# Kernel optimization log

Measured on AMD Instinct MI355X. Metric: run time of the kernel, lower is better.

## Reference

```python
import jax, jax.numpy as jnp
import numpy as np

B, R, C, COILS, SEGS, POL, PAD = 4, 256, 256, 32, 4, 2, 20


def _fft2c(x):
    # centered 2D FFT over axes (1,2) with 1/sqrt(R*C) norm (matches fft2c_coil_tf_buda)
    scale = 1.0 / np.sqrt(x.shape[1] * x.shape[2]).astype(np.float32)
    x = jnp.fft.fftshift(x, axes=(1, 2))
    x = jnp.fft.fft2(x, axes=(1, 2))
    return jnp.fft.fftshift(x, axes=(1, 2)) * scale


def _ifft2c(x):
    # centered 2D IFFT over axes (1,2) with sqrt(R*C) norm (matches ifft2c_coil_tf_buda)
    scale = np.sqrt(x.shape[1] * x.shape[2]).astype(np.float32)
    x = jnp.fft.ifftshift(x, axes=(1, 2))
    x = jnp.fft.ifft2(x, axes=(1, 2))
    return jnp.fft.ifftshift(x, axes=(1, 2)) * scale


def _center_crop(x, h, w):
    oh = (x.shape[1] - h) // 2
    ow = (x.shape[2] - w) // 2
    return x[:, oh:oh + h, ow:ow + w]


def _center_pad(x, h, w):
    ph = h - x.shape[1]
    pw = w - x.shape[2]
    pads = [(0, 0), (ph // 2, ph - ph // 2), (pw // 2, pw - pw // 2), (0, 0)]
    return jnp.pad(x, pads)


def setup_inputs() -> dict:
    key = jax.random.key(0)
    ks = jax.random.split(key, 7)
    return {
        "x_re": jax.random.normal(ks[0], (B, R + PAD, C + PAD, POL), jnp.float32),
        "x_im": jax.random.normal(ks[1], (B, R + PAD, C + PAD, POL), jnp.float32),
        "csm_re": jax.random.normal(ks[2], (B, R, C, COILS), jnp.float32),
        "csm_im": jax.random.normal(ks[3], (B, R, C, COILS), jnp.float32),
        "wmap_re": jax.random.normal(ks[4], (B, R, C, POL, SEGS), jnp.float32),
        "wmap_im": jax.random.normal(ks[5], (B, R, C, POL, SEGS), jnp.float32),
        "mask": jax.random.randint(ks[6], (B, R, C, POL, SEGS), 0, 2).astype(jnp.float32),
        "num_rows": R, "num_cols": C, "num_coils": COILS,
        "num_segs": SEGS, "num_polarities": POL,
    }


def reference(x_re, x_im, csm_re, csm_im, wmap_re, wmap_im, mask,
              num_rows, num_cols, num_coils, num_segs, num_polarities):
    x = (x_re + 1j * x_im).astype(jnp.complex64)
    csm = (csm_re + 1j * csm_im).astype(jnp.complex64)      # [B,R,C,coil]
    wmap = (wmap_re + 1j * wmap_im).astype(jnp.complex64)   # [B,R,C,pol,seg]

    # ---- forward model A ----
    img = _center_crop(x, num_rows, num_cols)                # [B,R,C,pol]
    # broadcast instead of tf.tile: [B,R,C,coil,pol,seg]
    tmp_i = (img[:, :, :, None, :, None]
             * wmap[:, :, :, None, :, :]
             * csm[:, :, :, :, None, None])
    tmp_k = _fft2c(tmp_i)
    kspace = jnp.sum(tmp_k * mask[:, :, :, None, :, :], axis=-1)  # [B,R,C,coil,pol]

    # ---- adjoint model A^H ----
    tk = kspace[..., None] * mask[:, :, :, None, :, :]       # [B,R,C,coil,pol,seg]
    ti = _ifft2c(tk)
    ti = ti * jnp.conj(wmap)[:, :, :, None, :, :] * jnp.conj(csm)[:, :, :, :, None, None]
    out = jnp.sum(ti, axis=(3, 5))                           # sum coils and segments -> [B,R,C,pol]

    out = _center_pad(out, num_rows + PAD, num_rows + PAD)   # tf pads both dims with num_rows+20
    return jnp.stack([out.real, out.imag], axis=-1)          # [B,R+20,R+20,pol,2]
```

## Files before the change

### kernel.cpp

```cpp
#include <hip/hip_runtime.h>
#include <hip/hip_fp16.h>

#define NB 4
#define NR 256
#define NC 256
#define NCOIL 32
#define NSEG 4
#define NPOL 2
#define OD 276
#define OFF 10
#define NCC 16

typedef float2 c32;

__device__ __forceinline__ c32 cmul(c32 a, c32 b){
  return make_float2(a.x*b.x - a.y*b.y, a.x*b.y + a.y*b.x);
}
__device__ __forceinline__ c32 cmulj(c32 a, c32 b){
  return make_float2(a.x*b.x + a.y*b.y, a.y*b.x - a.x*b.y);
}
__device__ __forceinline__ int pd(int a){ return a + (a >> 4); }

__device__ __forceinline__ void wsync(){ __builtin_amdgcn_wave_barrier(); }

__device__ __forceinline__ void init_tab(c32* tab, int tid){
  float th = (float)tid * 0.0245436926061703f;
  float sn, cs;
  sincosf(th, &sn, &cs);
  tab[tid] = make_float2(cs, -sn);
}

template<int DIR>
__device__ __forceinline__ void fft256(const c32* xin, c32* xout,
                                       c32* b0, c32* b1, const c32* tab, int u){
  c32* bufs[2] = { b0, b1 };
  #pragma unroll
  for (int s = 0; s < 4; ++s){
    const int m = 1 << (2*s);
    c32 a0, a1, a2, a3;
    if (s == 0){ a0 = xin[0]; a1 = xin[1]; a2 = xin[2]; a3 = xin[3]; }
    else {
      const c32* src = bufs[(s+1)&1];
      a0 = src[pd(u)]; a1 = src[pd(u+64)]; a2 = src[pd(u+128)]; a3 = src[pd(u+192)];
    }
    c32 s0 = make_float2(a0.x+a2.x, a0.y+a2.y);
    c32 d0 = make_float2(a0.x-a2.x, a0.y-a2.y);
    c32 s1 = make_float2(a1.x+a3.x, a1.y+a3.y);
    c32 d1 = make_float2(a1.x-a3.x, a1.y-a3.y);
    c32 X0 = make_float2(s0.x+s1.x, s0.y+s1.y);
    c32 X2 = make_float2(s0.x-s1.x, s0.y-s1.y);
    c32 X1, X3;
    if (DIR > 0){
      X1 = make_float2(d0.x + d1.y, d0.y - d1.x);
      X3 = make_float2(d0.x - d1.y, d0.y + d1.x);
    } else {
      X1 = make_float2(d0.x - d1.y, d0.y + d1.x);
      X3 = make_float2(d0.x + d1.y, d0.y - d1.x);
    }
    int e1 = u & ~(m-1);
    c32 w1 = tab[e1];
    c32 w2 = tab[(2*e1) & 255];
    c32 w3 = tab[(3*e1) & 255];
    if (DIR < 0){ w1.y = -w1.y; w2.y = -w2.y; w3.y = -w3.y; }
    X1 = cmul(X1, w1); X2 = cmul(X2, w2); X3 = cmul(X3, w3);
    if (s == 3){
      xout[0] = X0; xout[1] = X1; xout[2] = X2; xout[3] = X3;
    } else {
      c32* dst = bufs[s&1];
      int j = u >> (2*s);
      int k = u & (m-1);
      int base = k + 4*m*j;
      dst[pd(base)]      = X0;
      dst[pd(base+m)]    = X1;
      dst[pd(base+2*m)]  = X2;
      dst[pd(base+3*m)]  = X3;
    }
    wsync();
  }
}

__global__ __launch_bounds__(256) void zero_kernel(float* __restrict__ out, int n){
  int i = blockIdx.x*256 + threadIdx.x;
  if (i < n) out[i] = 0.0f;
}

__global__ __launch_bounds__(256) void pack_common_kernel(
    int b0,
    const float* __restrict__ x_re, const float* __restrict__ x_im,
    const float* __restrict__ wm_re, const float* __restrict__ wm_im,
    const float* __restrict__ mask,
    c32* __restrict__ img_t, c32* __restrict__ w_t, float* __restrict__ m_t)
{
  int r = blockIdx.x & (NR-1);
  int bl = blockIdx.x >> 8;
  int b = b0 + bl;
  int c = threadIdx.x;
  const size_t PL = (size_t)NR*NC;
  float sc = (((r + c) & 1) ? -1.0f : 1.0f) * (1.0f/256.0f);
  size_t xrow = (((size_t)b*OD) + (r+OFF))*OD + (c+OFF);
  #pragma unroll
  for (int pol = 0; pol < NPOL; ++pol){
    size_t xi = xrow*NPOL + pol;
    img_t[((size_t)(bl*NPOL+pol))*PL + (size_t)r*NC + c] =
        make_float2(x_re[xi]*sc, x_im[xi]*sc);
  }
  size_t wbase = (((size_t)b*NR + r)*NC + c)*(NPOL*NSEG);
  const float4* wre4 = (const float4*)&wm_re[wbase];
  const float4* wim4 = (const float4*)&wm_im[wbase];
  const float4* mk4  = (const float4*)&mask[wbase];
  #pragma unroll
  for (int pol = 0; pol < NPOL; ++pol){
    float4 re = wre4[pol], im = wim4[pol], mk = mk4[pol];
    float rr[4] = {re.x, re.y, re.z, re.w};
    float ii[4] = {im.x, im.y, im.z, im.w};
    float mm[4] = {mk.x, mk.y, mk.z, mk.w};
    #pragma unroll
    for (int seg = 0; seg < NSEG; ++seg){
      int ps = bl*(NPOL*NSEG) + pol*NSEG + seg;
      w_t[(size_t)ps*PL + (size_t)r*NC + c] = make_float2(rr[seg], ii[seg]);
      m_t[(size_t)ps*PL + (size_t)c*NR + r] = mm[seg];
    }
  }
}

__global__ __launch_bounds__(256) void pack_csm_kernel(
    int b,
    const float* __restrict__ csm_re, const float* __restrict__ csm_im,
    c32* __restrict__ c_t)
{
  int r = blockIdx.x;
  int c = threadIdx.x;
  const size_t PL = (size_t)NR*NC;
  size_t base = (((size_t)b*NR + r)*NC + c)*NCOIL;
  c32* cp = c_t + (size_t)r*NC + c;
  for (int cl = 0; cl < NCOIL; cl += 4){
    float4 re = *(const float4*)&csm_re[base + cl];
    float4 im = *(const float4*)&csm_im[base + cl];
    cp[(size_t)(cl+0)*PL] = make_float2(re.x, im.x);
    cp[(size_t)(cl+1)*PL] = make_float2(re.y, im.y);
    cp[(size_t)(cl+2)*PL] = make_float2(re.z, im.z);
    cp[(size_t)(cl+3)*PL] = make_float2(re.w, im.w);
  }
}

__global__ __launch_bounds__(256) void stageA_kernel(
    const c32* __restrict__ img_t, const c32* __restrict__ w_t,
    const c32* __restrict__ c_t, __half2* __restrict__ T1)
{
  __shared__ c32 tab[256];
  __shared__ c32 fbuf[4][2][272];
  __shared__ __half2 tile[NC*17];
  int tid = threadIdx.x;
  int u = tid & 63, w = tid >> 6;
  init_tab(tab, tid);
  __syncthreads();
  int bid = blockIdx.x;
  int p  = bid >> 4;
  int rt = bid & 15;
  int seg = p & 3, pol = (p>>2) & 1, cl = p >> 3;

  for (int ri = 0; ri < 4; ++ri){
    int rl = w*4 + ri;
    int r = rt*16 + rl;
    const c32* ir = img_t + ((size_t)pol*NR + r)*NC;
    const c32* wr = w_t  + ((size_t)(pol*NSEG+seg)*NR + r)*NC;
    const c32* cr = c_t  + ((size_t)cl*NR + r)*NC;
    c32 xin[4], xout[4];
    #pragma unroll
    for (int i = 0; i < 4; ++i){
      int c = u + 64*i;
      xin[i] = cmul(cmul(ir[c], wr[c]), cr[c]);
    }
    fft256<1>(xin, xout, fbuf[w][0], fbuf[w][1], tab, u);
    #pragma unroll
    for (int t = 0; t < 4; ++t){
      int c = u + 64*t;
      tile[c*17 + rl] = __floats2half2_rn(xout[t].x, xout[t].y);
    }
  }
  __syncthreads();
  __half2* tp = T1 + (size_t)p*(NR*NC);
  int r0 = rt*16;
  #pragma unroll
  for (int cb = 0; cb < 16; ++cb){
    int cc = w*64 + cb*4 + (u >> 4);
    int rl = u & 15;
    tp[cc*NR + r0 + rl] = tile[cc*17 + rl];
  }
}

__global__ __launch_bounds__(256) void stageB_kernel(
    const __half2* __restrict__ T1, const float* __restrict__ m_t,
    __half2* __restrict__ T2)
{
  __shared__ c32 tab[256];
  __shared__ c32 fbuf[4][2][272];
  __shared__ __half2 tile[16][256];
  int tid = threadIdx.x, u = tid & 63, w = tid >> 6;
  init_tab(tab, tid);
  __syncthreads();
  int bid = blockIdx.x;
  int ct = bid & 15;
  int g  = bid >> 4;
  int pol = g & 1;
  int c0 = ct*16;
  const size_t PL = (size_t)NR*NC;

  c32 K[4][4];
  #pragma unroll
  for (int j = 0; j < 4; ++j)
    #pragma unroll
    for (int t = 0; t < 4; ++t) K[j][t] = make_float2(0.f, 0.f);

  #pragma unroll
  for (int j = 0; j < 4; ++j){
    int col = c0 + w*4 + j;
    #pragma unroll 1
    for (int seg = 0; seg < NSEG; ++seg){
      const __half2* tp = T1 + ((size_t)(g*NSEG+seg))*PL + (size_t)col*NR;
      const float*  mp = m_t + ((size_t)(pol*NSEG+seg))*PL + (size_t)col*NR;
      c32 xin[4], xout[4];
      float mv[4];
      #pragma unroll
      for (int i = 0; i < 4; ++i){
        xin[i] = __half22float2(tp[u + 64*i]);
        mv[i]  = mp[u + 64*i];
      }
      fft256<1>(xin, xout, fbuf[w][0], fbuf[w][1], tab, u);
      #pragma unroll
      for (int t = 0; t < 4; ++t){
        K[j][t].x += mv[t]*xout[t].x;
        K[j][t].y += mv[t]*xout[t].y;
      }
    }
  }
  #pragma unroll 1
  for (int seg = 0; seg < NSEG; ++seg){
    #pragma unroll
    for (int j = 0; j < 4; ++j){
      int col = c0 + w*4 + j;
      const float* mp = m_t + ((size_t)(pol*NSEG+seg))*PL + (size_t)col*NR;
      c32 xin[4], xout[4];
      #pragma unroll
      for (int t = 0; t < 4; ++t){
        float mv = mp[u + 64*t];
        xin[t] = make_float2(K[j][t].x*mv, K[j][t].y*mv);
      }
      fft256<-1>(xin, xout, fbuf[w][0], fbuf[w][1], tab, u);
      #pragma unroll
      for (int t = 0; t < 4; ++t)
        tile[w*4+j][u + 64*t] = __floats2half2_rn(xout[t].x*(1.0f/256.0f),
                                                  xout[t].y*(1.0f/256.0f));
    }
    __syncthreads();
    {
      int r = tid;
      unsigned pk[16];
      #pragma unroll
      for (int k = 0; k < 16; ++k){
        __half2 h = tile[k][r];
        pk[k] = *(unsigned*)&h;
      }
      uint4* dst = (uint4*)(T2 + ((size_t)(g*NSEG+seg))*PL + (size_t)r*NC + c0);
      dst[0] = make_uint4(pk[0],  pk[1],  pk[2],  pk[3]);
      dst[1] = make_uint4(pk[4],  pk[5],  pk[6],  pk[7]);
      dst[2] = make_uint4(pk[8],  pk[9],  pk[10], pk[11]);
      dst[3] = make_uint4(pk[12], pk[13], pk[14], pk[15]);
    }
    __syncthreads();
  }
}

__global__ __launch_bounds__(256) void stageC_part_kernel(
    const __half2* __restrict__ T2, const c32* __restrict__ w_t,
    const c32* __restrict__ c_t, __half2* __restrict__ part, int ch0)
{
  __shared__ c32 tab[256];
  __shared__ c32 fbuf[4][2][272];
  int tid = threadIdx.x, u = tid & 63, w = tid >> 6;
  init_tab(tab, tid);
  __syncthreads();
  int bid = blockIdx.x;
  int rq = bid & 63, pol = (bid>>6) & 1, ch = bid >> 7;
  int r = rq*4 + w;
  const size_t PL = (size_t)NR*NC;

  c32 acc[4];
  #pragma unroll
  for (int t = 0; t < 4; ++t) acc[t] = make_float2(0.f, 0.f);

  __half2 v[4];
  {
    const __half2* rp = T2 + ((size_t)((ch*2*NPOL+pol)*NSEG))*PL + (size_t)r*NC;
    #pragma unroll
    for (int i = 0; i < 4; ++i) v[i] = rp[u + 64*i];
  }
  #pragma unroll 1
  for (int pl = 0; pl < 2*NSEG; ++pl){
    int cl = ch*2 + (pl>>2), seg = pl & 3;
    c32 xin[4], xout[4];
    #pragma unroll
    for (int i = 0; i < 4; ++i) xin[i] = __half22float2(v[i]);
    if (pl < 2*NSEG-1){
      int cl2 = ch*2 + ((pl+1)>>2), seg2 = (pl+1) & 3;
      const __half2* rp = T2 + ((size_t)((cl2*NPOL+pol)*NSEG+seg2))*PL + (size_t)r*NC;
      #pragma unroll
      for (int i = 0; i < 4; ++i) v[i] = rp[u + 64*i];
    }
    fft256<-1>(xin, xout, fbuf[w][0], fbuf[w][1], tab, u);
    const c32* wr = w_t + ((size_t)(pol*NSEG+seg)*NR + r)*NC;
    const c32* cr = c_t + ((size_t)cl*NR + r)*NC;
    #pragma unroll
    for (int t = 0; t < 4; ++t){
      int cp = u + 64*t;
      c32 vv = cmulj(xout[t], wr[cp]);
      vv = cmulj(vv, cr[cp]);
      acc[t].x += vv.x;
      acc[t].y += vv.y;
    }
  }
  __half2* pp = part + ((size_t)((ch0+ch)*NPOL+pol))*PL + (size_t)r*NC;
  #pragma unroll
  for (int t = 0; t < 4; ++t)
    pp[u + 64*t] = __floats2half2_rn(acc[t].x, acc[t].y);
}

__global__ __launch_bounds__(256) void reduceC_kernel(
    int b, const __half2* __restrict__ part, float* __restrict__ out)
{
  int r = blockIdx.x, c = threadIdx.x;
  const size_t PL = (size_t)NR*NC;
  float2 s[NPOL];
  #pragma unroll
  for (int pol = 0; pol < NPOL; ++pol) s[pol] = make_float2(0.f, 0.f);
  #pragma unroll 4
  for (int ch = 0; ch < NCC; ++ch){
    #pragma unroll
    for (int pol = 0; pol < NPOL; ++pol){
      float2 f = __half22float2(part[((size_t)(ch*NPOL+pol))*PL + (size_t)r*NC + c]);
      s[pol].x += f.x; s[pol].y += f.y;
    }
  }
  float sgn = ((r + c) & 1) ? -1.0f : 1.0f;
  float4 o = make_float4(sgn*s[0].x, sgn*s[0].y, sgn*s[1].x, sgn*s[1].y);
  size_t oidx = (((size_t)b*OD + (r+OFF))*OD + (c+OFF));
  ((float4*)out)[oidx] = o;
}

extern "C" void kernel_launch(void* const* d_in, const int* in_sizes, int n_in,
                              void* d_out, int out_size, void* d_ws, size_t ws_size,
                              hipStream_t stream)
{
  (void)in_sizes; (void)n_in;
  const float* x_re   = (const float*)d_in[0];
  const float* x_im   = (const float*)d_in[1];
  const float* csm_re = (const float*)d_in[2];
  const float* csm_im = (const float*)d_in[3];
  const float* wm_re  = (const float*)d_in[4];
  const float* wm_im  = (const float*)d_in[5];
  const float* mask   = (const float*)d_in[6];

  const size_t PL = (size_t)NR*NC;
  const size_t imgB1 = (size_t)NPOL*PL*sizeof(c32);
  const size_t wB1   = (size_t)NPOL*NSEG*PL*sizeof(c32);
  const size_t mB1   = (size_t)NPOL*NSEG*PL*sizeof(float);
  const size_t csmB1 = (size_t)NCOIL*PL*sizeof(c32);
  const size_t partB = (size_t)NCC*NPOL*PL*4;
  const size_t coilB = (size_t)NPOL*NSEG*PL*4;

  const size_t fixed = NB*(imgB1 + wB1 + mB1) + csmB1 + partB;

  int CH = 32;
  while (CH > 4){
    if (fixed + (size_t)CH*2*coilB <= ws_size) break;
    CH >>= 1;
  }

  char* ws = (char*)d_ws;
  c32* img_t = (c32*)ws;
  c32* w_t   = (c32*)(ws + NB*imgB1);
  float* m_t = (float*)(ws + NB*(imgB1 + wB1));
  c32* c_t   = (c32*)(ws + NB*(imgB1 + wB1 + mB1));
  __half2* part = (__half2*)(ws + NB*(imgB1 + wB1 + mB1) + csmB1);
  __half2* T1 = (__half2*)(ws + fixed);
  __half2* T2 = (__half2*)(ws + fixed + (size_t)CH*coilB);

  float* out = (float*)d_out;
  zero_kernel<<<(out_size + 255)/256, 256, 0, stream>>>(out, out_size);

  pack_common_kernel<<<NB*NR, 256, 0, stream>>>(0, x_re, x_im, wm_re, wm_im,
                                                mask, img_t, w_t, m_t);
  for (int b = 0; b < NB; ++b){
    c32* img_b = img_t + (size_t)b*NPOL*PL;
    c32* w_b   = w_t   + (size_t)b*NPOL*NSEG*PL;
    float* m_b = m_t   + (size_t)b*NPOL*NSEG*PL;
    pack_csm_kernel<<<NR, 256, 0, stream>>>(b, csm_re, csm_im, c_t);
    for (int c0 = 0; c0 < NCOIL; c0 += CH){
      c32* c_b = c_t + (size_t)c0*PL;
      stageA_kernel<<<CH*NPOL*NSEG*16, 256, 0, stream>>>(img_b, w_b, c_b, T1);
      stageB_kernel<<<CH*NPOL*16, 256, 0, stream>>>(T1, m_b, T2);
      stageC_part_kernel<<<(CH/2)*NPOL*64, 256, 0, stream>>>(T2, w_b, c_b,
                                                             part, c0/2);
    }
    reduceC_kernel<<<NR, 256, 0, stream>>>(b, part, out);
  }
}
```

Baseline: 596.3 us.

## Replace LDS-staged radix-4 FFT with register-resident shuffle FFT in bit-reversed order

Rewrites the 256-point FFT as one radix-4 stage in registers followed by six radix-2 stages done with cross-lane xor shuffles, so there are no shared-memory stage buffers and no twiddle table. The forward transform leaves its output in a permuted (digit-reversed) order and the inverse takes that order as input. The k-space mask is therefore stored in the same permuted order so the mask multiply between them stays correct. This removes LDS traffic, bank-conflict padding and block barriers from the FFT, at the cost of more sincos work per thread for twiddles and many shuffle instructions.

Result: slower. 733.2 us (+23.0%).

```diff
diff --git a/kernel.cpp b/kernel.cpp
--- a/kernel.cpp
+++ b/kernel.cpp
@@ -19,64 +19,81 @@
 __device__ __forceinline__ c32 cmulj(c32 a, c32 b){
   return make_float2(a.x*b.x + a.y*b.y, a.y*b.x - a.x*b.y);
 }
-__device__ __forceinline__ int pd(int a){ return a + (a >> 4); }
-
-__device__ __forceinline__ void wsync(){ __builtin_amdgcn_wave_barrier(); }
-
-__device__ __forceinline__ void init_tab(c32* tab, int tid){
-  float th = (float)tid * 0.0245436926061703f;
+
+
+struct Twid { c32 f4[3]; c32 f[6]; };
+
+__device__ __forceinline__ void make_tw(int u, Twid& T){
   float sn, cs;
-  sincosf(th, &sn, &cs);
-  tab[tid] = make_float2(cs, -sn);
-}
-
-template<int DIR>
-__device__ __forceinline__ void fft256(const c32* xin, c32* xout,
-                                       c32* b0, c32* b1, const c32* tab, int u){
-  c32* bufs[2] = { b0, b1 };
-  #pragma unroll
-  for (int s = 0; s < 4; ++s){
-    const int m = 1 << (2*s);
-    c32 a0, a1, a2, a3;
-    if (s == 0){ a0 = xin[0]; a1 = xin[1]; a2 = xin[2]; a3 = xin[3]; }
-    else {
-      const c32* src = bufs[(s+1)&1];
-      a0 = src[pd(u)]; a1 = src[pd(u+64)]; a2 = src[pd(u+128)]; a3 = src[pd(u+192)];
-    }
-    c32 s0 = make_float2(a0.x+a2.x, a0.y+a2.y);
-    c32 d0 = make_float2(a0.x-a2.x, a0.y-a2.y);
-    c32 s1 = make_float2(a1.x+a3.x, a1.y+a3.y);
-    c32 d1 = make_float2(a1.x-a3.x, a1.y-a3.y);
-    c32 X0 = make_float2(s0.x+s1.x, s0.y+s1.y);
-    c32 X2 = make_float2(s0.x-s1.x, s0.y-s1.y);
-    c32 X1, X3;
-    if (DIR > 0){
-      X1 = make_float2(d0.x + d1.y, d0.y - d1.x);
-      X3 = make_float2(d0.x - d1.y, d0.y + d1.x);
-    } else {
-      X1 = make_float2(d0.x - d1.y, d0.y + d1.x);
-      X3 = make_float2(d0.x + d1.y, d0.y - d1.x);
-    }
-    int e1 = u & ~(m-1);
-    c32 w1 = tab[e1];
-    c32 w2 = tab[(2*e1) & 255];
-    c32 w3 = tab[(3*e1) & 255];
-    if (DIR < 0){ w1.y = -w1.y; w2.y = -w2.y; w3.y = -w3.y; }
-    X1 = cmul(X1, w1); X2 = cmul(X2, w2); X3 = cmul(X3, w3);
-    if (s == 3){
-      xout[0] = X0; xout[1] = X1; xout[2] = X2; xout[3] = X3;
-    } else {
-      c32* dst = bufs[s&1];
-      int j = u >> (2*s);
-      int k = u & (m-1);
-      int base = k + 4*m*j;
-      dst[pd(base)]      = X0;
-      dst[pd(base+m)]    = X1;
-      dst[pd(base+2*m)]  = X2;
-      dst[pd(base+3*m)]  = X3;
-    }
-    wsync();
-  }
+  sincosf(0.024543692606170260f * (float)u, &sn, &cs);
+  T.f4[0] = make_float2(cs, -sn);
+  T.f4[1] = cmul(T.f4[0], T.f4[0]);
+  T.f4[2] = cmul(T.f4[1], T.f4[0]);
+  #pragma unroll
+  for (int s = 0; s < 6; ++s){
+    const int d = 32 >> s;
+    int e = (u & d) ? (u & (d-1)) : 0;
+    float ang = 3.14159265358979323846f * (float)e / (float)d;
+    sincosf(ang, &sn, &cs);
+    T.f[s] = make_float2(cs, -sn);
+  }
+}
+
+__device__ __forceinline__ c32 shflx(c32 v, int m){
+  return make_float2(__shfl_xor(v.x, m, 64), __shfl_xor(v.y, m, 64));
+}
+
+__device__ __forceinline__ void fft256_fwd(c32* x, const Twid& T, int u){
+  c32 a  = make_float2(x[0].x+x[2].x, x[0].y+x[2].y);
+  c32 b  = make_float2(x[0].x-x[2].x, x[0].y-x[2].y);
+  c32 c  = make_float2(x[1].x+x[3].x, x[1].y+x[3].y);
+  c32 dd = make_float2(x[1].x-x[3].x, x[1].y-x[3].y);
+  x[0] = make_float2(a.x+c.x, a.y+c.y);
+  x[2] = cmul(make_float2(a.x-c.x, a.y-c.y), T.f4[1]);
+  x[1] = cmul(make_float2(b.x+dd.y, b.y-dd.x), T.f4[0]);
+  x[3] = cmul(make_float2(b.x-dd.y, b.y+dd.x), T.f4[2]);
+  #pragma unroll
+  for (int s = 0; s < 6; ++s){
+    const int d = 32 >> s;
+    #pragma unroll
+    for (int j = 0; j < 4; ++j){
+      c32 o = shflx(x[j], d);
+      c32 t;
+      if (u & d){ t.x = o.x - x[j].x; t.y = o.y - x[j].y; }
+      else      { t.x = x[j].x + o.x; t.y = x[j].y + o.y; }
+      x[j] = cmul(t, T.f[s]);
+    }
+  }
+}
+
+__device__ __forceinline__ void fft256_inv(c32* x, const Twid& T, int u){
+  #pragma unroll
+  for (int s = 0; s < 6; ++s){
+    const int d = 1 << s;
+    #pragma unroll
+    for (int j = 0; j < 4; ++j){
+      c32 vt = cmulj(x[j], T.f[5-s]);
+      c32 o = shflx(vt, d);
+      if (u & d){ x[j].x = o.x - vt.x; x[j].y = o.y - vt.y; }
+      else      { x[j].x = vt.x + o.x; x[j].y = vt.y + o.y; }
+    }
+  }
+  x[1] = cmulj(x[1], T.f4[0]);
+  x[2] = cmulj(x[2], T.f4[1]);
+  x[3] = cmulj(x[3], T.f4[2]);
+  c32 a  = make_float2(x[0].x+x[2].x, x[0].y+x[2].y);
+  c32 b  = make_float2(x[0].x-x[2].x, x[0].y-x[2].y);
+  c32 c  = make_float2(x[1].x+x[3].x, x[1].y+x[3].y);
+  c32 dd = make_float2(x[1].x-x[3].x, x[1].y-x[3].y);
+  x[0] = make_float2(a.x+c.x, a.y+c.y);
+  x[2] = make_float2(a.x-c.x, a.y-c.y);
+  x[1] = make_float2(b.x-dd.y, b.y+dd.x);
+  x[3] = make_float2(b.x+dd.y, b.y-dd.x);
+}
+
+__device__ __forceinline__ int pinv(int k){
+  int r6 = (int)(__brev((unsigned)(k >> 2)) >> 26);
+  return ((k & 3) << 6) | r6;
 }
 
 __global__ __launch_bounds__(256) void zero_kernel(float* __restrict__ out, int n){
@@ -104,6 +121,7 @@
     img_t[((size_t)(bl*NPOL+pol))*PL + (size_t)r*NC + c] =
         make_float2(x_re[xi]*sc, x_im[xi]*sc);
   }
+  int rs = pinv(r), cs = pinv(c);
   size_t wbase = (((size_t)b*NR + r)*NC + c)*(NPOL*NSEG);
   const float4* wre4 = (const float4*)&wm_re[wbase];
   const float4* wim4 = (const float4*)&wm_im[wbase];
@@ -118,7 +136,7 @@
     for (int seg = 0; seg < NSEG; ++seg){
       int ps = bl*(NPOL*NSEG) + pol*NSEG + seg;
       w_t[(size_t)ps*PL + (size_t)r*NC + c] = make_float2(rr[seg], ii[seg]);
-      m_t[(size_t)ps*PL + (size_t)c*NR + r] = mm[seg];
+      m_t[(size_t)ps*PL + (size_t)cs*NR + rs] = mm[seg];
     }
   }
 }
@@ -147,35 +165,33 @@
     const c32* __restrict__ img_t, const c32* __restrict__ w_t,
     const c32* __restrict__ c_t, __half2* __restrict__ T1)
 {
-  __shared__ c32 tab[256];
-  __shared__ c32 fbuf[4][2][272];
   __shared__ __half2 tile[NC*17];
   int tid = threadIdx.x;
   int u = tid & 63, w = tid >> 6;
-  init_tab(tab, tid);
-  __syncthreads();
+  Twid T; make_tw(u, T);
   int bid = blockIdx.x;
   int p  = bid >> 4;
   int rt = bid & 15;
   int seg = p & 3, pol = (p>>2) & 1, cl = p >> 3;
 
+  #pragma unroll 1
   for (int ri = 0; ri < 4; ++ri){
     int rl = w*4 + ri;
     int r = rt*16 + rl;
     const c32* ir = img_t + ((size_t)pol*NR + r)*NC;
     const c32* wr = w_t  + ((size_t)(pol*NSEG+seg)*NR + r)*NC;
     const c32* cr = c_t  + ((size_t)cl*NR + r)*NC;
-    c32 xin[4], xout[4];
+    c32 x[4];
     #pragma unroll
     for (int i = 0; i < 4; ++i){
       int c = u + 64*i;
-      xin[i] = cmul(cmul(ir[c], wr[c]), cr[c]);
-    }
-    fft256<1>(xin, xout, fbuf[w][0], fbuf[w][1], tab, u);
+      x[i] = cmul(cmul(ir[c], wr[c]), cr[c]);
+    }
+    fft256_fwd(x, T, u);
     #pragma unroll
     for (int t = 0; t < 4; ++t){
       int c = u + 64*t;
-      tile[c*17 + rl] = __floats2half2_rn(xout[t].x, xout[t].y);
+      tile[c*17 + rl] = __floats2half2_rn(x[t].x, x[t].y);
     }
   }
   __syncthreads();
@@ -193,12 +209,9 @@
     const __half2* __restrict__ T1, const float* __restrict__ m_t,
     __half2* __restrict__ T2)
 {
-  __shared__ c32 tab[256];
-  __shared__ c32 fbuf[4][2][272];
   __shared__ __half2 tile[16][256];
   int tid = threadIdx.x, u = tid & 63, w = tid >> 6;
-  init_tab(tab, tid);
-  __syncthreads();
+  Twid T; make_tw(u, T);
   int bid = blockIdx.x;
   int ct = bid & 15;
   int g  = bid >> 4;
@@ -219,18 +232,18 @@
     for (int seg = 0; seg < NSEG; ++seg){
       const __half2* tp = T1 + ((size_t)(g*NSEG+seg))*PL + (size_t)col*NR;
       const float*  mp = m_t + ((size_t)(pol*NSEG+seg))*PL + (size_t)col*NR;
-      c32 xin[4], xout[4];
+      c32 x[4];
       float mv[4];
       #pragma unroll
       for (int i = 0; i < 4; ++i){
-        xin[i] = __half22float2(tp[u + 64*i]);
-        mv[i]  = mp[u + 64*i];
+        x[i]  = __half22float2(tp[u + 64*i]);
+        mv[i] = mp[u + 64*i];
       }
-      fft256<1>(xin, xout, fbuf[w][0], fbuf[w][1], tab, u);
+      fft256_fwd(x, T, u);
       #pragma unroll
       for (int t = 0; t < 4; ++t){
-        K[j][t].x += mv[t]*xout[t].x;
-        K[j][t].y += mv[t]*xout[t].y;
+        K[j][t].x += mv[t]*x[t].x;
+        K[j][t].y += mv[t]*x[t].y;
       }
     }
   }
@@ -240,17 +253,17 @@
     for (int j = 0; j < 4; ++j){
       int col = c0 + w*4 + j;
       const float* mp = m_t + ((size_t)(pol*NSEG+seg))*PL + (size_t)col*NR;
-      c32 xin[4], xout[4];
+      c32 x[4];
       #pragma unroll
       for (int t = 0; t < 4; ++t){
         float mv = mp[u + 64*t];
-        xin[t] = make_float2(K[j][t].x*mv, K[j][t].y*mv);
+        x[t] = make_float2(K[j][t].x*mv, K[j][t].y*mv);
       }
-      fft256<-1>(xin, xout, fbuf[w][0], fbuf[w][1], tab, u);
+      fft256_inv(x, T, u);
       #pragma unroll
       for (int t = 0; t < 4; ++t)
-        tile[w*4+j][u + 64*t] = __floats2half2_rn(xout[t].x*(1.0f/256.0f),
-                                                  xout[t].y*(1.0f/256.0f));
+        tile[w*4+j][u + 64*t] = __floats2half2_rn(x[t].x*(1.0f/256.0f),
+                                                  x[t].y*(1.0f/256.0f));
     }
     __syncthreads();
     {
@@ -275,11 +288,8 @@
     const __half2* __restrict__ T2, const c32* __restrict__ w_t,
     const c32* __restrict__ c_t, __half2* __restrict__ part, int ch0)
 {
-  __shared__ c32 tab[256];
-  __shared__ c32 fbuf[4][2][272];
   int tid = threadIdx.x, u = tid & 63, w = tid >> 6;
-  init_tab(tab, tid);
-  __syncthreads();
+  Twid T; make_tw(u, T);
   int bid = blockIdx.x;
   int rq = bid & 63, pol = (bid>>6) & 1, ch = bid >> 7;
   int r = rq*4 + w;
@@ -298,22 +308,22 @@
   #pragma unroll 1
   for (int pl = 0; pl < 2*NSEG; ++pl){
     int cl = ch*2 + (pl>>2), seg = pl & 3;
-    c32 xin[4], xout[4];
-    #pragma unroll
-    for (int i = 0; i < 4; ++i) xin[i] = __half22float2(v[i]);
+    c32 x[4];
+    #pragma unroll
+    for (int i = 0; i < 4; ++i) x[i] = __half22float2(v[i]);
     if (pl < 2*NSEG-1){
       int cl2 = ch*2 + ((pl+1)>>2), seg2 = (pl+1) & 3;
       const __half2* rp = T2 + ((size_t)((cl2*NPOL+pol)*NSEG+seg2))*PL + (size_t)r*NC;
       #pragma unroll
       for (int i = 0; i < 4; ++i) v[i] = rp[u + 64*i];
     }
-    fft256<-1>(xin, xout, fbuf[w][0], fbuf[w][1], tab, u);
+    fft256_inv(x, T, u);
     const c32* wr = w_t + ((size_t)(pol*NSEG+seg)*NR + r)*NC;
     const c32* cr = c_t + ((size_t)cl*NR + r)*NC;
     #pragma unroll
     for (int t = 0; t < 4; ++t){
       int cp = u + 64*t;
-      c32 vv = cmulj(xout[t], wr[cp]);
+      c32 vv = cmulj(x[t], wr[cp]);
       vv = cmulj(vv, cr[cp]);
       acc[t].x += vv.x;
       acc[t].y += vv.y;
```

## Use permuted FFT data ordering for vectorized transposes, register twiddles, half-precision mask

Applied to the files above, without the earlier changes.

The FFT now works in place and keeps its twiddle factors in registers, computed with sincosf at kernel start, instead of reading them from a shared-memory table. The intermediate T1 and the mask are stored in a digit-permuted row order, so stage B can read each FFT input as one contiguous 16-byte vector per thread and stage A can write its transposed output as uint4 stores. The mask is stored as fp16 to cut its memory traffic. Stage C now preloads its wmap and csm operands before the inverse FFT so those loads overlap the transform. The costs are higher register pressure, repeated sincos work in every block, and the accuracy risk of fp16 mask storage, although the mask values are only 0 and 1.

Result: slower. 687.7 us (+15.3%).

```diff
diff --git a/kernel.cpp b/kernel.cpp
--- a/kernel.cpp
+++ b/kernel.cpp
@@ -20,27 +20,34 @@
   return make_float2(a.x*b.x + a.y*b.y, a.y*b.x - a.x*b.y);
 }
 __device__ __forceinline__ int pd(int a){ return a + (a >> 4); }
-
 __device__ __forceinline__ void wsync(){ __builtin_amdgcn_wave_barrier(); }
 
-__device__ __forceinline__ void init_tab(c32* tab, int tid){
-  float th = (float)tid * 0.0245436926061703f;
-  float sn, cs;
-  sincosf(th, &sn, &cs);
-  tab[tid] = make_float2(cs, -sn);
+__device__ __forceinline__ int pord(int r){ return 4*(r & 63) + (r >> 6); }
+
+struct TW { c32 t1[4]; c32 t2[4]; c32 t3[4]; };
+__device__ __forceinline__ void mk_tw(int u, TW& T){
+  #pragma unroll
+  for (int s = 0; s < 4; ++s){
+    int e = u & ~((1 << (2*s)) - 1);
+    float a = -0.0245436926061703f * (float)e;
+    float sn, cs; sincosf(a, &sn, &cs);
+    c32 w1 = make_float2(cs, sn);
+    T.t1[s] = w1;
+    T.t2[s] = cmul(w1, w1);
+    T.t3[s] = cmul(T.t2[s], w1);
+  }
 }
 
 template<int DIR>
-__device__ __forceinline__ void fft256(const c32* xin, c32* xout,
-                                       c32* b0, c32* b1, const c32* tab, int u){
-  c32* bufs[2] = { b0, b1 };
+__device__ __forceinline__ void fft256(c32* x, c32* b0, c32* b1,
+                                       const TW& T, int u){
   #pragma unroll
   for (int s = 0; s < 4; ++s){
     const int m = 1 << (2*s);
     c32 a0, a1, a2, a3;
-    if (s == 0){ a0 = xin[0]; a1 = xin[1]; a2 = xin[2]; a3 = xin[3]; }
+    if (s == 0){ a0 = x[0]; a1 = x[1]; a2 = x[2]; a3 = x[3]; }
     else {
-      const c32* src = bufs[(s+1)&1];
+      const c32* src = ((s & 1) ? b0 : b1);
       a0 = src[pd(u)]; a1 = src[pd(u+64)]; a2 = src[pd(u+128)]; a3 = src[pd(u+192)];
     }
     c32 s0 = make_float2(a0.x+a2.x, a0.y+a2.y);
@@ -57,16 +64,13 @@
       X1 = make_float2(d0.x - d1.y, d0.y + d1.x);
       X3 = make_float2(d0.x + d1.y, d0.y - d1.x);
     }
-    int e1 = u & ~(m-1);
-    c32 w1 = tab[e1];
-    c32 w2 = tab[(2*e1) & 255];
-    c32 w3 = tab[(3*e1) & 255];
+    c32 w1 = T.t1[s], w2 = T.t2[s], w3 = T.t3[s];
     if (DIR < 0){ w1.y = -w1.y; w2.y = -w2.y; w3.y = -w3.y; }
     X1 = cmul(X1, w1); X2 = cmul(X2, w2); X3 = cmul(X3, w3);
     if (s == 3){
-      xout[0] = X0; xout[1] = X1; xout[2] = X2; xout[3] = X3;
+      x[0] = X0; x[1] = X1; x[2] = X2; x[3] = X3;
     } else {
-      c32* dst = bufs[s&1];
+      c32* dst = ((s & 1) ? b1 : b0);
       int j = u >> (2*s);
       int k = u & (m-1);
       int base = k + 4*m*j;
@@ -85,26 +89,25 @@
 }
 
 __global__ __launch_bounds__(256) void pack_common_kernel(
-    int b0,
     const float* __restrict__ x_re, const float* __restrict__ x_im,
     const float* __restrict__ wm_re, const float* __restrict__ wm_im,
     const float* __restrict__ mask,
-    c32* __restrict__ img_t, c32* __restrict__ w_t, float* __restrict__ m_t)
+    c32* __restrict__ img_t, c32* __restrict__ w_t, __half* __restrict__ m_t)
 {
   int r = blockIdx.x & (NR-1);
   int bl = blockIdx.x >> 8;
-  int b = b0 + bl;
   int c = threadIdx.x;
   const size_t PL = (size_t)NR*NC;
   float sc = (((r + c) & 1) ? -1.0f : 1.0f) * (1.0f/256.0f);
-  size_t xrow = (((size_t)b*OD) + (r+OFF))*OD + (c+OFF);
+  size_t xrow = (((size_t)bl*OD) + (r+OFF))*OD + (c+OFF);
   #pragma unroll
   for (int pol = 0; pol < NPOL; ++pol){
     size_t xi = xrow*NPOL + pol;
     img_t[((size_t)(bl*NPOL+pol))*PL + (size_t)r*NC + c] =
         make_float2(x_re[xi]*sc, x_im[xi]*sc);
   }
-  size_t wbase = (((size_t)b*NR + r)*NC + c)*(NPOL*NSEG);
+  int pr = pord(r);
+  size_t wbase = (((size_t)bl*NR + r)*NC + c)*(NPOL*NSEG);
   const float4* wre4 = (const float4*)&wm_re[wbase];
   const float4* wim4 = (const float4*)&wm_im[wbase];
   const float4* mk4  = (const float4*)&mask[wbase];
@@ -118,7 +121,7 @@
     for (int seg = 0; seg < NSEG; ++seg){
       int ps = bl*(NPOL*NSEG) + pol*NSEG + seg;
       w_t[(size_t)ps*PL + (size_t)r*NC + c] = make_float2(rr[seg], ii[seg]);
-      m_t[(size_t)ps*PL + (size_t)c*NR + r] = mm[seg];
+      m_t[((size_t)ps*NC + c)*NR + pr] = __float2half(mm[seg]);
     }
   }
 }
@@ -147,63 +150,61 @@
     const c32* __restrict__ img_t, const c32* __restrict__ w_t,
     const c32* __restrict__ c_t, __half2* __restrict__ T1)
 {
-  __shared__ c32 tab[256];
   __shared__ c32 fbuf[4][2][272];
   __shared__ __half2 tile[NC*17];
   int tid = threadIdx.x;
   int u = tid & 63, w = tid >> 6;
-  init_tab(tab, tid);
-  __syncthreads();
+  TW T; mk_tw(u, T);
   int bid = blockIdx.x;
   int p  = bid >> 4;
   int rt = bid & 15;
   int seg = p & 3, pol = (p>>2) & 1, cl = p >> 3;
 
+  #pragma unroll 1
   for (int ri = 0; ri < 4; ++ri){
-    int rl = w*4 + ri;
-    int r = rt*16 + rl;
+    int r = 4*rt + w + 64*ri;
+    int klocal = 4*w + ri;
     const c32* ir = img_t + ((size_t)pol*NR + r)*NC;
     const c32* wr = w_t  + ((size_t)(pol*NSEG+seg)*NR + r)*NC;
     const c32* cr = c_t  + ((size_t)cl*NR + r)*NC;
-    c32 xin[4], xout[4];
+    c32 x[4];
     #pragma unroll
     for (int i = 0; i < 4; ++i){
       int c = u + 64*i;
-      xin[i] = cmul(cmul(ir[c], wr[c]), cr[c]);
-    }
-    fft256<1>(xin, xout, fbuf[w][0], fbuf[w][1], tab, u);
-    #pragma unroll
-    for (int t = 0; t < 4; ++t){
-      int c = u + 64*t;
-      tile[c*17 + rl] = __floats2half2_rn(xout[t].x, xout[t].y);
-    }
+      x[i] = cmul(cmul(ir[c], wr[c]), cr[c]);
+    }
+    fft256<1>(x, fbuf[w][0], fbuf[w][1], T, u);
+    #pragma unroll
+    for (int t = 0; t < 4; ++t)
+      tile[(u + 64*t)*17 + klocal] = __floats2half2_rn(x[t].x, x[t].y);
   }
   __syncthreads();
-  __half2* tp = T1 + (size_t)p*(NR*NC);
-  int r0 = rt*16;
-  #pragma unroll
-  for (int cb = 0; cb < 16; ++cb){
-    int cc = w*64 + cb*4 + (u >> 4);
-    int rl = u & 15;
-    tp[cc*NR + r0 + rl] = tile[cc*17 + rl];
+  int a = tid >> 2, m = tid & 3;
+  #pragma unroll
+  for (int k = 0; k < 4; ++k){
+    int cc = a + 64*k;
+    __half2 h0 = tile[cc*17 + 4*m + 0];
+    __half2 h1 = tile[cc*17 + 4*m + 1];
+    __half2 h2 = tile[cc*17 + 4*m + 2];
+    __half2 h3 = tile[cc*17 + 4*m + 3];
+    uint4 pk = make_uint4(*(unsigned*)&h0, *(unsigned*)&h1,
+                          *(unsigned*)&h2, *(unsigned*)&h3);
+    *(uint4*)(T1 + (size_t)p*(NR*NC) + (size_t)cc*NR + 16*rt + 4*m) = pk;
   }
 }
 
 __global__ __launch_bounds__(256) void stageB_kernel(
-    const __half2* __restrict__ T1, const float* __restrict__ m_t,
+    const __half2* __restrict__ T1, const __half* __restrict__ m_t,
     __half2* __restrict__ T2)
 {
-  __shared__ c32 tab[256];
   __shared__ c32 fbuf[4][2][272];
   __shared__ __half2 tile[16][256];
   int tid = threadIdx.x, u = tid & 63, w = tid >> 6;
-  init_tab(tab, tid);
-  __syncthreads();
+  TW T; mk_tw(u, T);
   int bid = blockIdx.x;
   int ct = bid & 15;
   int g  = bid >> 4;
   int pol = g & 1;
-  int c0 = ct*16;
   const size_t PL = (size_t)NR*NC;
 
   c32 K[4][4];
@@ -212,45 +213,56 @@
     #pragma unroll
     for (int t = 0; t < 4; ++t) K[j][t] = make_float2(0.f, 0.f);
 
-  #pragma unroll
+  #pragma unroll 1
   for (int j = 0; j < 4; ++j){
-    int col = c0 + w*4 + j;
-    #pragma unroll 1
+    int col = 4*ct + w + 64*j;
+    uint4 dj[4]; uint2 mj[4];
+    #pragma unroll
     for (int seg = 0; seg < NSEG; ++seg){
-      const __half2* tp = T1 + ((size_t)(g*NSEG+seg))*PL + (size_t)col*NR;
-      const float*  mp = m_t + ((size_t)(pol*NSEG+seg))*PL + (size_t)col*NR;
-      c32 xin[4], xout[4];
-      float mv[4];
+      dj[seg] = *(const uint4*)(T1 + ((size_t)(g*NSEG+seg))*PL
+                                + (size_t)col*NR + 4*u);
+      mj[seg] = *(const uint2*)(m_t + ((size_t)(pol*NSEG+seg)*NC + col)*NR + 4*u);
+    }
+    #pragma unroll
+    for (int seg = 0; seg < NSEG; ++seg){
+      c32 x[4]; float mv[4];
+      const __half2* hp = (const __half2*)&dj[seg];
+      const __half*  mp = (const __half*)&mj[seg];
       #pragma unroll
       for (int i = 0; i < 4; ++i){
-        xin[i] = __half22float2(tp[u + 64*i]);
-        mv[i]  = mp[u + 64*i];
+        x[i]  = __half22float2(hp[i]);
+        mv[i] = __half2float(mp[i]);
       }
-      fft256<1>(xin, xout, fbuf[w][0], fbuf[w][1], tab, u);
+      fft256<1>(x, fbuf[w][0], fbuf[w][1], T, u);
       #pragma unroll
       for (int t = 0; t < 4; ++t){
-        K[j][t].x += mv[t]*xout[t].x;
-        K[j][t].y += mv[t]*xout[t].y;
+        K[j][t].x += mv[t]*x[t].x;
+        K[j][t].y += mv[t]*x[t].y;
       }
     }
   }
   #pragma unroll 1
   for (int seg = 0; seg < NSEG; ++seg){
+    uint2 mj[4];
     #pragma unroll
     for (int j = 0; j < 4; ++j){
-      int col = c0 + w*4 + j;
-      const float* mp = m_t + ((size_t)(pol*NSEG+seg))*PL + (size_t)col*NR;
-      c32 xin[4], xout[4];
+      int col = 4*ct + w + 64*j;
+      mj[j] = *(const uint2*)(m_t + ((size_t)(pol*NSEG+seg)*NC + col)*NR + 4*u);
+    }
+    #pragma unroll
+    for (int j = 0; j < 4; ++j){
+      c32 x[4];
+      const __half* mp = (const __half*)&mj[j];
       #pragma unroll
       for (int t = 0; t < 4; ++t){
-        float mv = mp[u + 64*t];
-        xin[t] = make_float2(K[j][t].x*mv, K[j][t].y*mv);
+        float mv = __half2float(mp[t]);
+        x[t] = make_float2(K[j][t].x*mv, K[j][t].y*mv);
       }
-      fft256<-1>(xin, xout, fbuf[w][0], fbuf[w][1], tab, u);
+      fft256<-1>(x, fbuf[w][0], fbuf[w][1], T, u);
       #pragma unroll
       for (int t = 0; t < 4; ++t)
-        tile[w*4+j][u + 64*t] = __floats2half2_rn(xout[t].x*(1.0f/256.0f),
-                                                  xout[t].y*(1.0f/256.0f));
+        tile[4*w+j][u + 64*t] = __floats2half2_rn(x[t].x*(1.0f/256.0f),
+                                                  x[t].y*(1.0f/256.0f));
     }
     __syncthreads();
     {
@@ -261,7 +273,8 @@
         __half2 h = tile[k][r];
         pk[k] = *(unsigned*)&h;
       }
-      uint4* dst = (uint4*)(T2 + ((size_t)(g*NSEG+seg))*PL + (size_t)r*NC + c0);
+      uint4* dst = (uint4*)(T2 + ((size_t)(g*NSEG+seg))*PL
+                            + (size_t)r*NC + 16*ct);
       dst[0] = make_uint4(pk[0],  pk[1],  pk[2],  pk[3]);
       dst[1] = make_uint4(pk[4],  pk[5],  pk[6],  pk[7]);
       dst[2] = make_uint4(pk[8],  pk[9],  pk[10], pk[11]);
@@ -275,11 +288,9 @@
     const __half2* __restrict__ T2, const c32* __restrict__ w_t,
     const c32* __restrict__ c_t, __half2* __restrict__ part, int ch0)
 {
-  __shared__ c32 tab[256];
   __shared__ c32 fbuf[4][2][272];
   int tid = threadIdx.x, u = tid & 63, w = tid >> 6;
-  init_tab(tab, tid);
-  __syncthreads();
+  TW T; mk_tw(u, T);
   int bid = blockIdx.x;
   int rq = bid & 63, pol = (bid>>6) & 1, ch = bid >> 7;
   int r = rq*4 + w;
@@ -289,32 +300,30 @@
   #pragma unroll
   for (int t = 0; t < 4; ++t) acc[t] = make_float2(0.f, 0.f);
 
-  __half2 v[4];
-  {
-    const __half2* rp = T2 + ((size_t)((ch*2*NPOL+pol)*NSEG))*PL + (size_t)r*NC;
-    #pragma unroll
-    for (int i = 0; i < 4; ++i) v[i] = rp[u + 64*i];
-  }
+  uint4 v = *(const uint4*)(T2 + ((size_t)((ch*2*NPOL+pol)*NSEG))*PL
+                            + (size_t)r*NC + 4*u);
   #pragma unroll 1
   for (int pl = 0; pl < 2*NSEG; ++pl){
     int cl = ch*2 + (pl>>2), seg = pl & 3;
-    c32 xin[4], xout[4];
-    #pragma unroll
-    for (int i = 0; i < 4; ++i) xin[i] = __half22float2(v[i]);
+    c32 x[4];
+    const __half2* hp = (const __half2*)&v;
+    #pragma unroll
+    for (int i = 0; i < 4; ++i) x[i] = __half22float2(hp[i]);
     if (pl < 2*NSEG-1){
       int cl2 = ch*2 + ((pl+1)>>2), seg2 = (pl+1) & 3;
-      const __half2* rp = T2 + ((size_t)((cl2*NPOL+pol)*NSEG+seg2))*PL + (size_t)r*NC;
-      #pragma unroll
-      for (int i = 0; i < 4; ++i) v[i] = rp[u + 64*i];
-    }
-    fft256<-1>(xin, xout, fbuf[w][0], fbuf[w][1], tab, u);
+      v = *(const uint4*)(T2 + ((size_t)((cl2*NPOL+pol)*NSEG+seg2))*PL
+                          + (size_t)r*NC + 4*u);
+    }
     const c32* wr = w_t + ((size_t)(pol*NSEG+seg)*NR + r)*NC;
     const c32* cr = c_t + ((size_t)cl*NR + r)*NC;
+    c32 wv[4], cv[4];
+    #pragma unroll
+    for (int t = 0; t < 4; ++t){ wv[t] = wr[u + 64*t]; cv[t] = cr[u + 64*t]; }
+    fft256<-1>(x, fbuf[w][0], fbuf[w][1], T, u);
     #pragma unroll
     for (int t = 0; t < 4; ++t){
-      int cp = u + 64*t;
-      c32 vv = cmulj(xout[t], wr[cp]);
-      vv = cmulj(vv, cr[cp]);
+      c32 vv = cmulj(x[t], wv[t]);
+      vv = cmulj(vv, cv[t]);
       acc[t].x += vv.x;
       acc[t].y += vv.y;
     }
@@ -363,7 +372,7 @@
   const size_t PL = (size_t)NR*NC;
   const size_t imgB1 = (size_t)NPOL*PL*sizeof(c32);
   const size_t wB1   = (size_t)NPOL*NSEG*PL*sizeof(c32);
-  const size_t mB1   = (size_t)NPOL*NSEG*PL*sizeof(float);
+  const size_t mB1   = (size_t)NPOL*NSEG*PL*sizeof(__half);
   const size_t csmB1 = (size_t)NCOIL*PL*sizeof(c32);
   const size_t partB = (size_t)NCC*NPOL*PL*4;
   const size_t coilB = (size_t)NPOL*NSEG*PL*4;
@@ -379,7 +388,7 @@
   char* ws = (char*)d_ws;
   c32* img_t = (c32*)ws;
   c32* w_t   = (c32*)(ws + NB*imgB1);
-  float* m_t = (float*)(ws + NB*(imgB1 + wB1));
+  __half* m_t = (__half*)(ws + NB*(imgB1 + wB1));
   c32* c_t   = (c32*)(ws + NB*(imgB1 + wB1 + mB1));
   __half2* part = (__half2*)(ws + NB*(imgB1 + wB1 + mB1) + csmB1);
   __half2* T1 = (__half2*)(ws + fixed);
@@ -388,12 +397,12 @@
   float* out = (float*)d_out;
   zero_kernel<<<(out_size + 255)/256, 256, 0, stream>>>(out, out_size);
 
-  pack_common_kernel<<<NB*NR, 256, 0, stream>>>(0, x_re, x_im, wm_re, wm_im,
+  pack_common_kernel<<<NB*NR, 256, 0, stream>>>(x_re, x_im, wm_re, wm_im,
                                                 mask, img_t, w_t, m_t);
   for (int b = 0; b < NB; ++b){
     c32* img_b = img_t + (size_t)b*NPOL*PL;
     c32* w_b   = w_t   + (size_t)b*NPOL*NSEG*PL;
-    float* m_b = m_t   + (size_t)b*NPOL*NSEG*PL;
+    __half* m_b = m_t  + (size_t)b*NPOL*NSEG*PL;
     pack_csm_kernel<<<NR, 256, 0, stream>>>(b, csm_re, csm_im, c_t);
     for (int c0 = 0; c0 < NCOIL; c0 += CH){
       c32* c_b = c_t + (size_t)c0*PL;
```
